# Performance work log

Hardware: AMD Instinct MI355X
Metric: run time of the kernel (lower is better)

The kernel has to match this reference:

```python
import jax, jax.numpy as jnp
import numpy as np

HIDDEN = 1024
HEADS = 12
HEAD_DIM = 64
NEG = -1e12


def _rope(x):
    # x: [B, N, H, d], rotate along seq axis (axis 1), interleaved pairs
    B, N, H, d = x.shape
    inv_freq = 1.0 / (10000.0 ** (jnp.arange(0, d, 2, dtype=jnp.float32) / d))  # [d/2]
    pos = jnp.arange(N, dtype=jnp.float32)
    ang = pos[:, None] * inv_freq[None, :]                 # [N, d/2]
    sin = jnp.repeat(jnp.sin(ang), 2, axis=-1)[None, :, None, :]  # [1,N,1,d]
    cos = jnp.repeat(jnp.cos(ang), 2, axis=-1)[None, :, None, :]
    even = x[..., ::2]
    odd = x[..., 1::2]
    rot = jnp.stack([-odd, even], axis=-1).reshape(B, N, H, d)
    return x * cos + rot * sin


def setup_inputs() -> dict:
    key = jax.random.key(0)
    k1, k2, k3, k4 = jax.random.split(key, 4)
    hidden_states = jax.random.normal(k1, (16, 512, HIDDEN), dtype=jnp.float32)
    attention_weights = jax.random.randint(k2, (16, 512), 0, 2, dtype=jnp.int32)
    W = jax.random.normal(k3, (HIDDEN, HEADS * HEAD_DIM * 2), dtype=jnp.float32) * 0.02
    b = jax.random.normal(k4, (HEADS * HEAD_DIM * 2,), dtype=jnp.float32) * 0.02
    return {"hidden_states": hidden_states, "attention_weights": attention_weights, "W": W, "b": b}


def reference(hidden_states, attention_weights, W, b):
    B, N, _ = hidden_states.shape
    proj = hidden_states @ W + b                            # [B,N,H*2*d]
    proj = proj.reshape(B, N, HEADS, 2, HEAD_DIM)
    q, k = proj[..., 0, :], proj[..., 1, :]                 # [B,N,H,d]
    q = _rope(q)
    k = _rope(k)
    q = q / (HEAD_DIM ** 0.5)
    scores = jnp.einsum('bnhd,bmhd->bhnm', q, k)            # [B,H,N,N]
    # mask padded keys (key dim only, matching the torch repeat pattern)
    key_mask = (attention_weights == 0)[:, None, None, :]   # [B,1,1,N]
    scores = jnp.where(key_mask, NEG, scores)
    # mask diagonal
    diag = jnp.eye(N, dtype=bool)[None, None, :, :]
    scores = jnp.where(diag, NEG, scores)
    return jax.nn.sigmoid(scores)
```

## Files before the change

### kernel.cpp

```cpp
#include <hip/hip_runtime.h>

#define HEADS 12
#define HIDDEN 1024
#define NOUT 1536
#define SEQ 512

typedef __bf16 bf16x8 __attribute__((ext_vector_type(8)));
typedef float f32x4 __attribute__((ext_vector_type(4)));

__device__ __forceinline__ void gload_lds16(const void* g, void* l) {
  __builtin_amdgcn_global_load_lds(
      (const __attribute__((address_space(1))) unsigned int*)g,
      (__attribute__((address_space(3))) unsigned int*)l, 16, 0, 0);
}

__device__ __forceinline__ unsigned short f2bf(float f) {
  union { float f; unsigned u; } x;
  x.f = f;
  unsigned r = x.u + 0x7fffu + ((x.u >> 16) & 1u);
  return (unsigned short)(r >> 16);
}

__device__ __forceinline__ int swz8(int b, int per) {
  return (b & 7) * per + (b >> 3);
}

__global__ __launch_bounds__(256) void k_prep(const float* __restrict__ hidden,
                                              unsigned short* __restrict__ hidA,
                                              const float* __restrict__ W,
                                              unsigned short* __restrict__ Wt,
                                              float2* __restrict__ trig) {
  __shared__ unsigned short t[32][33];
  const int bid = blockIdx.x;
  const int tid = threadIdx.x;
  if (bid < 8192) {
    int i = bid * 256 + tid;
    float4 v = ((const float4*)hidden)[i];
    ushort4 o;
    o.x = f2bf(v.x); o.y = f2bf(v.y); o.z = f2bf(v.z); o.w = f2bf(v.w);
    ((ushort4*)hidA)[i] = o;
  } else if (bid < 8192 + 1536) {
    int tt = bid - 8192;
    int n0 = (tt % 48) * 32;
    int k0 = (tt / 48) * 32;
    int tx = tid & 31;
    int ty = tid >> 5;
#pragma unroll
    for (int i = 0; i < 4; ++i) {
      int k = k0 + ty + i * 8;
      t[ty + i * 8][tx] = f2bf(W[(size_t)k * NOUT + n0 + tx]);
    }
    __syncthreads();
#pragma unroll
    for (int i = 0; i < 4; ++i) {
      int n = n0 + ty + i * 8;
      Wt[(size_t)n * HIDDEN + k0 + tx] = t[tx][ty + i * 8];
    }
  } else {
    int i = (bid - 9728) * 256 + tid;
    int pos = i >> 5, j = i & 31;
    float inv = 1.0f / powf(10000.0f, (float)(2 * j) * (1.0f / 64.0f));
    float ang = (float)pos * inv;
    trig[i] = make_float2(cosf(ang), sinf(ang));
  }
}

__global__ __launch_bounds__(256, 3) void k_proj(const unsigned short* __restrict__ A,
                                                 const unsigned short* __restrict__ Bt,
                                                 const float* __restrict__ bias,
                                                 const float2* __restrict__ trig,
                                                 unsigned short* __restrict__ qb,
                                                 unsigned short* __restrict__ kb) {
  __shared__ unsigned short As[3][128 * 32];
  __shared__ unsigned short Bs[3][128 * 32];
  const int lin = swz8(blockIdx.x, 96);
  const int h = lin % 12;
  const int m0 = (lin / 12) * 128;
  const int n0 = h * 128;
  const int tid = threadIdx.x;
  const int wave = tid >> 6, lane = tid & 63;
  const int l15 = lane & 15, l4 = lane >> 4;
  const int wr = wave >> 1, wc = wave & 1;
  const int cchunk = (l4 ^ ((l15 >> 1) & 3)) * 8;

  const int c0 = tid, c1 = 256 + tid;
  const int r0 = c0 >> 2, r1 = c1 >> 2;
  const int s0 = ((c0 & 3) ^ ((r0 >> 1) & 3)) * 8;
  const int s1 = ((c1 & 3) ^ ((r1 >> 1) & 3)) * 8;
  const unsigned short* A0 = A + (size_t)(m0 + r0) * HIDDEN + s0;
  const unsigned short* A1 = A + (size_t)(m0 + r1) * HIDDEN + s1;
  const unsigned short* B0 = Bt + (size_t)(n0 + r0) * HIDDEN + s0;
  const unsigned short* B1 = Bt + (size_t)(n0 + r1) * HIDDEN + s1;

  f32x4 acc[4][4];
#pragma unroll
  for (int a = 0; a < 4; ++a)
#pragma unroll
    for (int b2 = 0; b2 < 4; ++b2) acc[a][b2] = (f32x4){0.f, 0.f, 0.f, 0.f};

#define STAGE(KT, BUF) do {                                   \
    const int kb_ = (KT) * 32;                                \
    gload_lds16(A0 + kb_, &As[BUF][c0 * 8]);                  \
    gload_lds16(A1 + kb_, &As[BUF][c1 * 8]);                  \
    gload_lds16(B0 + kb_, &Bs[BUF][c0 * 8]);                  \
    gload_lds16(B1 + kb_, &Bs[BUF][c1 * 8]);                  \
  } while (0)

#define STEP(KT, CUR, STG, DO_STAGE, VMC) do {                                         \
    if (DO_STAGE) STAGE((KT) + 2, STG);                                                \
    asm volatile("s_waitcnt vmcnt(" #VMC ")" ::: "memory");                            \
    __builtin_amdgcn_s_barrier();                                                      \
    bf16x8 af[4], bv[4];                                                               \
    const unsigned short* Ab_ = &As[CUR][0];                                           \
    const unsigned short* Bb_ = &Bs[CUR][0];                                           \
    _Pragma("unroll") for (int mi = 0; mi < 4; ++mi)                                   \
      af[mi] = *(const bf16x8*)(Ab_ + (wr * 64 + mi * 16 + l15) * 32 + cchunk);        \
    _Pragma("unroll") for (int ni = 0; ni < 4; ++ni)                                   \
      bv[ni] = *(const bf16x8*)(Bb_ + (wc * 64 + ni * 16 + l15) * 32 + cchunk);        \
    __builtin_amdgcn_s_setprio(1);                                                     \
    _Pragma("unroll") for (int mi = 0; mi < 4; ++mi)                                   \
      _Pragma("unroll") for (int ni = 0; ni < 4; ++ni)                                 \
        acc[mi][ni] = __builtin_amdgcn_mfma_f32_16x16x32_bf16(af[mi], bv[ni],          \
                                                              acc[mi][ni], 0, 0, 0);   \
    __builtin_amdgcn_s_setprio(0);                                                     \
    asm volatile("s_waitcnt lgkmcnt(0)" ::: "memory");                                 \
    __builtin_amdgcn_s_barrier();                                                      \
  } while (0)

  STAGE(0, 0);
  STAGE(1, 1);
  for (int t = 0; t < 30; t += 3) {
    STEP(t, 0, 2, true, 8);
    STEP(t + 1, 1, 0, true, 8);
    STEP(t + 2, 2, 1, true, 8);
  }
  STEP(30, 0, 0, false, 4);
  STEP(31, 1, 0, false, 0);
#undef STEP
#undef STAGE

#pragma unroll
  for (int ni = 0; ni < 4; ++ni) {
    const int c = wc * 64 + ni * 16 + l15;
    const int qk = c >> 6;
    const int d = c & 63;
    const int j = d >> 1;
    const int odd = d & 1;
    const float bias_v = bias[n0 + c];
    unsigned short* dst = qk ? kb : qb;
    const float scale = qk ? 1.0f : 0.125f;
#pragma unroll
    for (int mi = 0; mi < 4; ++mi) {
#pragma unroll
      for (int jj = 0; jj < 4; ++jj) {
        const int row = wr * 64 + mi * 16 + l4 * 4 + jj;
        const int m = m0 + row;
        const int bb = m >> 9, pos = m & 511;
        float v = acc[mi][ni][jj] + bias_v;
        float p = __shfl_xor(v, 1);
        float2 cs = trig[pos * 32 + j];
        float o = odd ? (v * cs.x + p * cs.y) : (v * cs.x - p * cs.y);
        o *= scale;
        dst[(((size_t)bb * HEADS + h) * SEQ + pos) * 64 + d] = f2bf(o);
      }
    }
  }
}

__global__ __launch_bounds__(256) void k_scores(const unsigned short* __restrict__ qb,
                                                const unsigned short* __restrict__ kb,
                                                const int* __restrict__ aw,
                                                float* __restrict__ out) {
  __shared__ unsigned short Qs[64 * 64];
  __shared__ unsigned short Ks[2][64 * 64];
  const int lin = swz8(blockIdx.x, 192);
  const int bh = lin >> 3;
  const int b = bh / HEADS;
  const int q0 = (lin & 7) * 64;
  const int tid = threadIdx.x;
  const int wave = tid >> 6, lane = tid & 63;
  const int l15 = lane & 15, l4 = lane >> 4;
  const int wkey = wave >> 1, wq = wave & 1;

  const unsigned short* qsrc = qb + (size_t)bh * SEQ * 64 + (size_t)q0 * 64;
  const unsigned short* ksrc = kb + (size_t)bh * SEQ * 64;

#pragma unroll
  for (int i = 0; i < 2; ++i) {
    int chunk = i * 256 + tid;
    gload_lds16(qsrc + chunk * 8, Qs + chunk * 8);
    gload_lds16(ksrc + chunk * 8, &Ks[0][chunk * 8]);
  }
  asm volatile("s_waitcnt vmcnt(0)" ::: "memory");
  __syncthreads();

  for (int tk = 0; tk < 8; ++tk) {
    const int cur = tk & 1;
    const int k0 = tk * 64;

    if (tk < 7) {
      const unsigned short* nsrc = ksrc + (size_t)(k0 + 64) * 64;
#pragma unroll
      for (int i = 0; i < 2; ++i) {
        int chunk = i * 256 + tid;
        gload_lds16(nsrc + chunk * 8, &Ks[cur ^ 1][chunk * 8]);
      }
    }

    f32x4 acc[2][2];
#pragma unroll
    for (int a = 0; a < 2; ++a)
#pragma unroll
      for (int b2 = 0; b2 < 2; ++b2) acc[a][b2] = (f32x4){0.f, 0.f, 0.f, 0.f};

#pragma unroll
    for (int kk = 0; kk < 2; ++kk) {
      bf16x8 kf[2], qf[2];
#pragma unroll
      for (int mi = 0; mi < 2; ++mi)
        kf[mi] = *(const bf16x8*)(&Ks[cur][0] + (wkey * 32 + mi * 16 + l15) * 64 + kk * 32 + l4 * 8);
#pragma unroll
      for (int ni = 0; ni < 2; ++ni)
        qf[ni] = *(const bf16x8*)(Qs + (wq * 32 + ni * 16 + l15) * 64 + kk * 32 + l4 * 8);
#pragma unroll
      for (int mi = 0; mi < 2; ++mi)
#pragma unroll
        for (int ni = 0; ni < 2; ++ni)
          acc[mi][ni] = __builtin_amdgcn_mfma_f32_16x16x32_bf16(kf[mi], qf[ni], acc[mi][ni], 0, 0, 0);
    }

#pragma unroll
    for (int mi = 0; mi < 2; ++mi) {
      const int keybase = k0 + wkey * 32 + mi * 16 + l4 * 4;
      const int4 aw4 = *(const int4*)(aw + b * SEQ + keybase);
#pragma unroll
      for (int ni = 0; ni < 2; ++ni) {
        const int nq = q0 + wq * 32 + ni * 16 + l15;
        f32x4 st;
        {
          float s0 = acc[mi][ni][0];
          st[0] = (aw4.x == 0 || nq == keybase + 0) ? 0.0f : 1.0f / (1.0f + __expf(-s0));
          float s1 = acc[mi][ni][1];
          st[1] = (aw4.y == 0 || nq == keybase + 1) ? 0.0f : 1.0f / (1.0f + __expf(-s1));
          float s2 = acc[mi][ni][2];
          st[2] = (aw4.z == 0 || nq == keybase + 2) ? 0.0f : 1.0f / (1.0f + __expf(-s2));
          float s3 = acc[mi][ni][3];
          st[3] = (aw4.w == 0 || nq == keybase + 3) ? 0.0f : 1.0f / (1.0f + __expf(-s3));
        }
        *(f32x4*)(out + (size_t)bh * SEQ * SEQ + (size_t)nq * SEQ + keybase) = st;
      }
    }

    __syncthreads();
  }
}

extern "C" void kernel_launch(void* const* d_in, const int* in_sizes, int n_in,
                              void* d_out, int out_size, void* d_ws, size_t ws_size,
                              hipStream_t stream) {
  const float* hidden = (const float*)d_in[0];
  const int* aw = (const int*)d_in[1];
  const float* W = (const float*)d_in[2];
  const float* bias = (const float*)d_in[3];
  float* out = (float*)d_out;

  char* ws = (char*)d_ws;
  unsigned short* hidA = (unsigned short*)ws;
  unsigned short* Wt = (unsigned short*)(ws + 16777216);
  unsigned short* qb = (unsigned short*)(ws + 19922944);
  unsigned short* kb = (unsigned short*)(ws + 32505856);
  float2* trig = (float2*)(ws + 45088768);

  k_prep<<<9792, 256, 0, stream>>>(hidden, hidA, W, Wt, trig);
  k_proj<<<768, 256, 0, stream>>>(hidA, Wt, bias, trig, qb, kb);
  k_scores<<<1536, 256, 0, stream>>>(qb, kb, aw, out);
}
```

Before: 106.4 us.

## Load Q/K fragments directly from global into registers in scores kernel

The scores kernel no longer stages Q and K tiles in LDS with double buffering and per-iteration barriers. Each wave now loads its Q fragments into registers once and, on every fully unrolled key-tile iteration, loads its K fragments straight from global memory. This removes LDS traffic and the per-tile __syncthreads. The cost is redundant global/L2 reads of K across waves and more register pressure. The kernel is dominated by the fp32 output writes, so the effect is likely small.

```diff
diff --git a/kernel.cpp b/kernel.cpp
--- a/kernel.cpp
+++ b/kernel.cpp
@@ -171,8 +171,6 @@
                                                 const unsigned short* __restrict__ kb,
                                                 const int* __restrict__ aw,
                                                 float* __restrict__ out) {
-  __shared__ unsigned short Qs[64 * 64];
-  __shared__ unsigned short Ks[2][64 * 64];
   const int lin = swz8(blockIdx.x, 192);
   const int bh = lin >> 3;
   const int b = bh / HEADS;
@@ -182,30 +180,28 @@
   const int l15 = lane & 15, l4 = lane >> 4;
   const int wkey = wave >> 1, wq = wave & 1;
 
-  const unsigned short* qsrc = qb + (size_t)bh * SEQ * 64 + (size_t)q0 * 64;
+  const unsigned short* qsrc = qb + (size_t)bh * SEQ * 64;
   const unsigned short* ksrc = kb + (size_t)bh * SEQ * 64;
 
-#pragma unroll
-  for (int i = 0; i < 2; ++i) {
-    int chunk = i * 256 + tid;
-    gload_lds16(qsrc + chunk * 8, Qs + chunk * 8);
-    gload_lds16(ksrc + chunk * 8, &Ks[0][chunk * 8]);
-  }
-  asm volatile("s_waitcnt vmcnt(0)" ::: "memory");
-  __syncthreads();
-
+  bf16x8 qf[2][2];
+#pragma unroll
+  for (int ni = 0; ni < 2; ++ni)
+#pragma unroll
+    for (int kk = 0; kk < 2; ++kk)
+      qf[ni][kk] = *(const bf16x8*)(qsrc + (size_t)(q0 + wq * 32 + ni * 16 + l15) * 64 +
+                                    kk * 32 + l4 * 8);
+
+#pragma unroll
   for (int tk = 0; tk < 8; ++tk) {
-    const int cur = tk & 1;
     const int k0 = tk * 64;
 
-    if (tk < 7) {
-      const unsigned short* nsrc = ksrc + (size_t)(k0 + 64) * 64;
-#pragma unroll
-      for (int i = 0; i < 2; ++i) {
-        int chunk = i * 256 + tid;
-        gload_lds16(nsrc + chunk * 8, &Ks[cur ^ 1][chunk * 8]);
-      }
-    }
+    bf16x8 kf[2][2];
+#pragma unroll
+    for (int mi = 0; mi < 2; ++mi)
+#pragma unroll
+      for (int kk = 0; kk < 2; ++kk)
+        kf[mi][kk] = *(const bf16x8*)(ksrc + (size_t)(k0 + wkey * 32 + mi * 16 + l15) * 64 +
+                                      kk * 32 + l4 * 8);
 
     f32x4 acc[2][2];
 #pragma unroll
@@ -214,20 +210,13 @@
       for (int b2 = 0; b2 < 2; ++b2) acc[a][b2] = (f32x4){0.f, 0.f, 0.f, 0.f};
 
 #pragma unroll
-    for (int kk = 0; kk < 2; ++kk) {
-      bf16x8 kf[2], qf[2];
+    for (int kk = 0; kk < 2; ++kk)
 #pragma unroll
       for (int mi = 0; mi < 2; ++mi)
-        kf[mi] = *(const bf16x8*)(&Ks[cur][0] + (wkey * 32 + mi * 16 + l15) * 64 + kk * 32 + l4 * 8);
-#pragma unroll
-      for (int ni = 0; ni < 2; ++ni)
-        qf[ni] = *(const bf16x8*)(Qs + (wq * 32 + ni * 16 + l15) * 64 + kk * 32 + l4 * 8);
-#pragma unroll
-      for (int mi = 0; mi < 2; ++mi)
 #pragma unroll
         for (int ni = 0; ni < 2; ++ni)
-          acc[mi][ni] = __builtin_amdgcn_mfma_f32_16x16x32_bf16(kf[mi], qf[ni], acc[mi][ni], 0, 0, 0);
-    }
+          acc[mi][ni] = __builtin_amdgcn_mfma_f32_16x16x32_bf16(kf[mi][kk], qf[ni][kk],
+                                                                acc[mi][ni], 0, 0, 0);
 
 #pragma unroll
     for (int mi = 0; mi < 2; ++mi) {
@@ -250,8 +239,6 @@
         *(f32x4*)(out + (size_t)bh * SEQ * SEQ + (size_t)nq * SEQ + keybase) = st;
       }
     }
-
-    __syncthreads();
   }
 }
 
```

Result: slower. 112.7 us (+5.8%).
